# Optimization experiments

Measured on AMD Instinct MI355X. Metric: run time of the kernel, lower is better.

Reference implementation:

```python
import jax, jax.numpy as jnp
import numpy as np

V, D, N, DK, DV, H, DFF = 32000, 512, 6, 64, 64, 8, 2048
B, S = 8, 512
EPS = 1e-5


def _pe(seq_len, d_model):
    pos = np.arange(seq_len)[:, None].astype(np.float32)
    i = np.arange(0, d_model, 2).astype(np.float32)
    ang = pos / np.power(10000.0, i / d_model)
    pe = np.zeros((seq_len, d_model), dtype=np.float32)
    pe[:, 0::2] = np.sin(ang)
    pe[:, 1::2] = np.cos(ang)
    return jnp.asarray(pe)


def _ln(x, g, b):
    m = jnp.mean(x, axis=-1, keepdims=True)
    v = jnp.mean(jnp.square(x - m), axis=-1, keepdims=True)
    return (x - m) * jax.lax.rsqrt(v + EPS) * g + b


def _mha(xq, xkv, Wq, Wk, Wv, bq, bk, bv, mask):
    # Wq/Wk: [H,D,DK], Wv: [H,D,DV]; mask: [B,Sq,Skv] additive
    q = jnp.einsum('bsd,hdk->bhsk', xq, Wq) + bq[None, :, None, :]
    k = jnp.einsum('bsd,hdk->bhsk', xkv, Wk) + bk[None, :, None, :]
    v = jnp.einsum('bsd,hdk->bhsk', xkv, Wv) + bv[None, :, None, :]
    scores = jnp.einsum('bhqk,bhsk->bhqs', q, k) / jnp.sqrt(jnp.float32(DK))
    scores = scores + mask[:, None, :, :]
    attn = jax.nn.softmax(scores, axis=-1)
    out = jnp.einsum('bhqs,bhsv->bhqv', attn, v)  # [B,H,Sq,DV]
    return out.transpose(0, 2, 1, 3).reshape(xq.shape[0], xq.shape[1], H * DV)


def setup_inputs() -> dict:
    key = jax.random.key(0)
    ks = jax.random.split(key, 24)
    sc = 0.02
    inp = {
        'decoder_input': jax.random.randint(ks[0], (B, S), 0, V),
        'encoder_output': jax.random.normal(ks[1], (B, S, D), dtype=jnp.float32),
        'self_mask': jnp.where(jnp.tril(jnp.ones((S, S), dtype=bool)), 0.0, -1e9)[None].repeat(B, 0).astype(jnp.float32),
        'cross_mask': jnp.zeros((B, S, S), dtype=jnp.float32),
        'emb': jax.random.normal(ks[2], (V, D), dtype=jnp.float32),
        'Wq_s': jax.random.normal(ks[3], (N, H, D, DK)) * sc,
        'Wk_s': jax.random.normal(ks[4], (N, H, D, DK)) * sc,
        'Wv_s': jax.random.normal(ks[5], (N, H, D, DV)) * sc,
        'bq_s': jnp.zeros((N, H, DK)), 'bk_s': jnp.zeros((N, H, DK)), 'bv_s': jnp.zeros((N, H, DV)),
        'Wq_c': jax.random.normal(ks[6], (N, H, D, DK)) * sc,
        'Wk_c': jax.random.normal(ks[7], (N, H, D, DK)) * sc,
        'Wv_c': jax.random.normal(ks[8], (N, H, D, DV)) * sc,
        'bq_c': jnp.zeros((N, H, DK)), 'bk_c': jnp.zeros((N, H, DK)), 'bv_c': jnp.zeros((N, H, DV)),
        'W1': jax.random.normal(ks[9], (N, D, DFF)) * sc,
        'b1': jnp.zeros((N, DFF)),
        'W2': jax.random.normal(ks[10], (N, DFF, D)) * sc,
        'b2': jnp.zeros((N, D)),
        'ln1_g': jnp.ones((N, D)), 'ln1_b': jnp.zeros((N, D)),
        'ln2_g': jnp.ones((N, D)), 'ln2_b': jnp.zeros((N, D)),
    }
    return inp


def reference(decoder_input, encoder_output, self_mask, cross_mask, emb,
              Wq_s, Wk_s, Wv_s, bq_s, bk_s, bv_s,
              Wq_c, Wk_c, Wv_c, bq_c, bk_c, bv_c,
              W1, b1, W2, b2, ln1_g, ln1_b, ln2_g, ln2_b):
    x = emb[decoder_input] + _pe(decoder_input.shape[1], D)[None]
    for l in range(N):
        sa = _mha(x, x, Wq_s[l], Wk_s[l], Wv_s[l], bq_s[l], bk_s[l], bv_s[l], self_mask)
        x = _ln(x + sa, ln1_g[l], ln1_b[l])
        ca = _mha(x, encoder_output, Wq_c[l], Wk_c[l], Wv_c[l], bq_c[l], bk_c[l], bv_c[l], cross_mask)
        x = _ln(x + ca, ln2_g[l], ln2_b[l])
        ff = jax.nn.relu(jnp.einsum('bsd,df->bsf', x, W1[l]) + b1[l])
        ff = jnp.einsum('bsf,fd->bsd', ff, W2[l]) + b2[l]
        # source reuses layer_norm2 for the third norm (layer_norm3 is dead)
        x = _ln(x + ff, ln2_g[l], ln2_b[l])
    return x
```

## Files before the change

### kernel.cpp

```cpp
#include <hip/hip_runtime.h>
#include <hip/hip_bf16.h>
#include <math.h>

#define BB 8
#define SS 512
#define DDIM 512
#define HH 8
#define DFFV 2048
#define NLAYER 6
#define EPSV 1e-5f

typedef __attribute__((ext_vector_type(8))) short bf16x8;
typedef __attribute__((ext_vector_type(4))) float f32x4;

static __device__ __forceinline__ ushort f2bf(float f) {
  union { float f; unsigned u; } uf; uf.f = f;
  unsigned u = uf.u;
  unsigned r = (u + 0x7fffu + ((u >> 16) & 1u)) >> 16;
  return (ushort)r;
}
static __device__ __forceinline__ float bf2f(ushort h) {
  union { unsigned u; float f; } x;
  x.u = ((unsigned)h) << 16;
  return x.f;
}

static __device__ __forceinline__ void gload_lds16(const void* g, void* l) {
  __builtin_amdgcn_global_load_lds(
      (const __attribute__((address_space(1))) void*)g,
      (__attribute__((address_space(3))) void*)l, 16, 0, 0);
}

__global__ __launch_bounds__(256) void embed_pe_kernel(
    const int* __restrict__ idx, const float* __restrict__ emb,
    ushort* __restrict__ xb) {
  int t = blockIdx.x * blockDim.x + threadIdx.x;
  if (t >= BB * SS * DDIM) return;
  int d = t & (DDIM - 1);
  int bs = t >> 9;
  int s = bs & (SS - 1);
  int tok = idx[bs];
  int i2 = d & ~1;
  float ang = (float)s * powf(10000.0f, -((float)i2) / (float)DDIM);
  float pe = (d & 1) ? cosf(ang) : sinf(ang);
  float v = emb[tok * DDIM + d] + pe;
  xb[t] = f2bf(v);
}

__global__ __launch_bounds__(256) void cast_bf16_kernel(
    const float* __restrict__ in, ushort* __restrict__ out, int n4) {
  int t = blockIdx.x * blockDim.x + threadIdx.x;
  if (t >= n4) return;
  float4 v = reinterpret_cast<const float4*>(in)[t];
  ushort4 o;
  o.x = f2bf(v.x); o.y = f2bf(v.y); o.z = f2bf(v.z); o.w = f2bf(v.w);
  reinterpret_cast<ushort4*>(out)[t] = o;
}

__global__ __launch_bounds__(256) void wtrans_kernel(
    const float* __restrict__ in, ushort* __restrict__ out, int R, int C,
    int lgH, size_t zl) {
  __shared__ float t[32][33];
  int z = blockIdx.z;
  int l = z >> lgH, hh = z & ((1 << lgH) - 1);
  const float* ip = in + (size_t)z * R * C;
  ushort* op = out + (size_t)l * zl + (size_t)hh * R * C;
  int j = threadIdx.x & 31, i0 = threadIdx.x >> 5;
  int r0 = blockIdx.y * 32, c0 = blockIdx.x * 32;
#pragma unroll
  for (int p = 0; p < 4; p++) {
    int r = r0 + i0 + p * 8;
    t[i0 + p * 8][j] = ip[(size_t)r * C + c0 + j];
  }
  __syncthreads();
#pragma unroll
  for (int p = 0; p < 4; p++) {
    int cc = c0 + i0 + p * 8;
    op[(size_t)cc * R + r0 + j] = f2bf(t[j][i0 + p * 8]);
  }
}

__global__ __launch_bounds__(256) void pack_bias_kernel(
    const float* __restrict__ bq, const float* __restrict__ bk,
    const float* __restrict__ bv, const float* __restrict__ bkc,
    const float* __restrict__ bvc, float* __restrict__ qkvb,
    float* __restrict__ ckvb) {
  int t = blockIdx.x * 256 + threadIdx.x;
  if (t < NLAYER * 1536) {
    int l = t / 1536, n = t % 1536;
    float v = n < 512 ? bq[l * 512 + n]
                      : (n < 1024 ? bk[l * 512 + n - 512] : bv[l * 512 + n - 1024]);
    qkvb[t] = v;
  }
  if (t < NLAYER * 1024) {
    int l = t / 1024, n = t % 1024;
    ckvb[t] = n < 512 ? bkc[l * 512 + n] : bvc[l * 512 + n - 512];
  }
}

template <int BM, int BN, int RELU, int OUTBF, int NTV, int LGP, int SPLITK>
__global__ __launch_bounds__(256) void gemm_mfma(
    const ushort* __restrict__ A, const ushort* __restrict__ Bw,
    const float* __restrict__ bias, float* __restrict__ Cf,
    ushort* __restrict__ Cb, ushort* __restrict__ vt, int M, int N, int K) {
  constexpr int WM = BM / 64;
  constexpr int WN = 4 / WM;
  constexpr int W = BN / WN;
  constexpr int AF = 4;
  constexpr int BF = W / 16;
  constexpr int GA = BM * 8;
  constexpr int GPT = (BM + BN) * 8 / 256;
  __shared__ __align__(16) ushort lds_s[2][(BM + BN) * 64];
  int bn = blockIdx.x * BN, bm = blockIdx.y * BM;
  int kz = (SPLITK > 1) ? blockIdx.z : 0;
  int Keff = K / SPLITK;
  int kbase = kz * Keff;
  int tid = threadIdx.x, lane = tid & 63, w = tid >> 6;
  int wm = w / WN, wn = w % WN;
  int c = lane & 15, g16 = lane >> 4;
  f32x4 acc[AF][BF] = {};

  auto STAGE = [&](int k0, int bufi) {
#pragma unroll
    for (int i = 0; i < GPT; i++) {
      int gidx = i * 256 + tid;
      int gbase = (i * 4 + w) * 64;
      const ushort* src;
      if (gidx < GA) {
        int row = gidx >> 3, dg = gidx & 7;
        src = A + (size_t)(bm + row) * K + kbase + k0 + ((dg ^ (row & 7)) << 3);
      } else {
        int bidx = gidx - GA;
        int row = bidx >> 3, dg = bidx & 7;
        src = Bw + (size_t)(bn + row) * K + kbase + k0 + ((dg ^ (row & 7)) << 3);
      }
      gload_lds16(src, (void*)((char*)(&lds_s[bufi][0]) + gbase * 16));
    }
  };

  int nk = Keff >> 6;
  STAGE(0, 0);
  for (int kt = 0; kt < nk; kt++) {
    int cur = kt & 1;
    if (kt + 1 < nk) {
      STAGE((kt + 1) << 6, cur ^ 1);
      asm volatile("s_waitcnt vmcnt(%0)" ::"n"(GPT) : "memory");
    } else {
      asm volatile("s_waitcnt vmcnt(0)" ::: "memory");
    }
    __builtin_amdgcn_s_barrier();
    __builtin_amdgcn_sched_barrier(0);
    const ushort* Alds = &lds_s[cur][0];
    const ushort* Blds = &lds_s[cur][BM * 64];
#pragma unroll
    for (int ks = 0; ks < 2; ks++) {
      int g = ks * 4 + g16;
      bf16x8 a[AF], b[BF];
#pragma unroll
      for (int i = 0; i < AF; i++) {
        int R = wm * 64 + i * 16 + c;
        a[i] = *(const bf16x8*)(Alds + R * 64 + ((g ^ (R & 7)) << 3));
      }
#pragma unroll
      for (int j = 0; j < BF; j++) {
        int Rb = wn * W + j * 16 + c;
        b[j] = *(const bf16x8*)(Blds + Rb * 64 + ((g ^ (Rb & 7)) << 3));
      }
#pragma unroll
      for (int i = 0; i < AF; i++)
#pragma unroll
        for (int j = 0; j < BF; j++)
          acc[i][j] = __builtin_amdgcn_mfma_f32_16x16x32_bf16(a[i], b[j],
                                                              acc[i][j], 0, 0, 0);
    }
    __builtin_amdgcn_sched_barrier(0);
    __builtin_amdgcn_s_barrier();
  }
  int rb = g16 * 4;
#pragma unroll
  for (int j = 0; j < BF; j++) {
    int col = bn + wn * W + j * 16 + c;
    float bv = (SPLITK > 1 && kz != 0) ? 0.0f : bias[col];
    int cc = LGP ? (col & ((1 << LGP) - 1)) : col;
    int lp = LGP ? (col >> LGP) : 0;
    if (NTV > 0 && cc >= NTV) {
      int hh = (cc - NTV) >> 6, dv = col & 63;
      ushort* vtl = vt + (size_t)lp * 2097152;
#pragma unroll
      for (int i = 0; i < AF; i++) {
        int row = bm + wm * 64 + i * 16 + rb;
        int b_ = row >> 9, s_ = row & 511;
        ushort4 o4;
        o4.x = f2bf(acc[i][j][0] + bv);
        o4.y = f2bf(acc[i][j][1] + bv);
        o4.z = f2bf(acc[i][j][2] + bv);
        o4.w = f2bf(acc[i][j][3] + bv);
        *reinterpret_cast<ushort4*>(
            vtl + ((size_t)(b_ * 8 + hh) * 64 + dv) * 512 + s_) = o4;
      }
    } else {
#pragma unroll
      for (int i = 0; i < AF; i++) {
#pragma unroll
        for (int qq = 0; qq < 4; qq++) {
          int row = bm + wm * 64 + i * 16 + rb + qq;
          float v = acc[i][j][qq] + bv;
          if (RELU) v = fmaxf(v, 0.0f);
          if (OUTBF)
            Cb[(size_t)row * N + col] = f2bf(v);
          else
            Cf[(size_t)kz * M * N + (size_t)row * N + col] = v;
        }
      }
    }
  }
}

template <int MASKED, int NW>
__global__ __launch_bounds__(NW * 64) void attn_mfma(
    const ushort* __restrict__ q, int qstr, const ushort* __restrict__ k,
    int kstr, const ushort* __restrict__ vt, ushort* __restrict__ out) {
  __shared__ __align__(16) char lds[32768 + NW * 2048];
  int q0 = blockIdx.x * (NW * 16), h = blockIdx.y, b = blockIdx.z;
  int tid = threadIdx.x, lane = tid & 63, w = tid >> 6;
  int c = lane & 15, g16 = lane >> 4, rb = g16 * 4;

  bf16x8 qa[2];
#pragma unroll
  for (int ks = 0; ks < 2; ks++)
    qa[ks] = *(const bf16x8*)(q + (size_t)(b * SS + q0 + 16 * w + c) * qstr +
                              h * 64 + ks * 32 + g16 * 8);
  f32x4 o[4] = {};
  float mrow[4], lrow[4];
#pragma unroll
  for (int j = 0; j < 4; j++) { mrow[j] = -1e30f; lrow[j] = 0.f; }

  int nt = MASKED ? (q0 >> 6) + 1 : 8;
  int pbase = 32768 + w * 2048;

  constexpr int GPTK = 512 / (NW * 64);
  bf16x8 rk[GPTK], rv[GPTK];
  const ushort* vbase = vt + ((size_t)(b * 8 + h) * 64) * 512;
  auto LOADT = [&](int kv0) {
#pragma unroll
    for (int i = 0; i < GPTK; i++) {
      int idx = tid + i * (NW * 64);
      int row = idx >> 3, gw = idx & 7;
      rk[i] = *(const bf16x8*)(k + (size_t)(b * SS + kv0 + row) * kstr +
                               h * 64 + gw * 8);
      rv[i] = *(const bf16x8*)(vbase + (size_t)row * 512 + kv0 + gw * 8);
    }
  };
  auto WRT = [&](int bufi) {
    char* p = lds + bufi * 16384;
#pragma unroll
    for (int i = 0; i < GPTK; i++) {
      int idx = tid + i * (NW * 64);
      int row = idx >> 3, gw = idx & 7;
      *(bf16x8*)(p + row * 128 + ((gw ^ (row & 7)) << 4)) = rk[i];
      *(bf16x8*)(p + 8192 + row * 128 + ((gw ^ (row & 7)) << 4)) = rv[i];
    }
  };
  LOADT(0);
  WRT(0);
  for (int t = 0; t < nt; t++) {
    if (t + 1 < nt) LOADT((t + 1) * 64);
    __syncthreads();
    char* kb_ = lds + (t & 1) * 16384;
    char* vb_ = kb_ + 8192;
    f32x4 s[4] = {};
    __builtin_amdgcn_s_setprio(1);
#pragma unroll
    for (int ks = 0; ks < 2; ks++) {
      int g = ks * 4 + g16;
#pragma unroll
      for (int f = 0; f < 4; f++) {
        int row = f * 16 + c;
        bf16x8 k8 = *(bf16x8*)(kb_ + row * 128 + ((g ^ (row & 7)) << 4));
        s[f] = __builtin_amdgcn_mfma_f32_16x16x32_bf16(qa[ks], k8, s[f], 0, 0, 0);
      }
    }
    __builtin_amdgcn_s_setprio(0);
    if (MASKED && t == nt - 1) {
#pragma unroll
      for (int f = 0; f < 4; f++)
#pragma unroll
        for (int j = 0; j < 4; j++)
          s[f][j] = s[f][j] * 0.125f +
                    ((f * 16 + c) <= (16 * w + rb + j) ? 0.0f : -1e9f);
    } else {
#pragma unroll
      for (int f = 0; f < 4; f++)
#pragma unroll
        for (int j = 0; j < 4; j++) s[f][j] *= 0.125f;
    }
#pragma unroll
    for (int j = 0; j < 4; j++) {
      float tm = fmaxf(fmaxf(s[0][j], s[1][j]), fmaxf(s[2][j], s[3][j]));
      tm = fmaxf(tm, __shfl_xor(tm, 1));
      tm = fmaxf(tm, __shfl_xor(tm, 2));
      tm = fmaxf(tm, __shfl_xor(tm, 4));
      tm = fmaxf(tm, __shfl_xor(tm, 8));
      float mn = fmaxf(mrow[j], tm);
      float sc = __expf(mrow[j] - mn);
      float p0 = __expf(s[0][j] - mn), p1 = __expf(s[1][j] - mn);
      float p2 = __expf(s[2][j] - mn), p3 = __expf(s[3][j] - mn);
      s[0][j] = p0; s[1][j] = p1; s[2][j] = p2; s[3][j] = p3;
      float ps = p0 + p1 + p2 + p3;
      ps += __shfl_xor(ps, 1);
      ps += __shfl_xor(ps, 2);
      ps += __shfl_xor(ps, 4);
      ps += __shfl_xor(ps, 8);
      lrow[j] = lrow[j] * sc + ps;
      mrow[j] = mn;
      o[0][j] *= sc; o[1][j] *= sc; o[2][j] *= sc; o[3][j] *= sc;
    }
#pragma unroll
    for (int f = 0; f < 4; f++) {
      int col = f * 16 + c;
      int cg = col >> 3, cb2 = (col & 7) * 2;
#pragma unroll
      for (int j = 0; j < 4; j++) {
        int r = rb + j;
        *(ushort*)(lds + pbase + r * 128 + ((cg ^ (r & 7)) << 4) + cb2) =
            f2bf(s[f][j]);
      }
    }
    __builtin_amdgcn_s_setprio(1);
#pragma unroll
    for (int ks2 = 0; ks2 < 2; ks2++) {
      int g = ks2 * 4 + g16;
      bf16x8 pa = *(bf16x8*)(lds + pbase + c * 128 + ((g ^ (c & 7)) << 4));
#pragma unroll
      for (int f = 0; f < 4; f++) {
        int row = f * 16 + c;
        bf16x8 v8 = *(bf16x8*)(vb_ + row * 128 + ((g ^ (row & 7)) << 4));
        o[f] = __builtin_amdgcn_mfma_f32_16x16x32_bf16(pa, v8, o[f], 0, 0, 0);
      }
    }
    __builtin_amdgcn_s_setprio(0);
    if (t + 1 < nt) WRT((t + 1) & 1);
  }
#pragma unroll
  for (int j = 0; j < 4; j++) {
    float inv = 1.0f / lrow[j];
    size_t rowo = (size_t)(b * SS + q0 + 16 * w + rb + j) * 512 + h * 64;
#pragma unroll
    for (int f = 0; f < 4; f++)
      out[rowo + f * 16 + c] = f2bf(o[f][j] * inv);
  }
}

template <int Y2>
__global__ __launch_bounds__(256) void add_ln_kernel(
    ushort* __restrict__ xb, const ushort* __restrict__ yb,
    const float* __restrict__ y0, const float* __restrict__ y1,
    const float* __restrict__ g, const float* __restrict__ bta,
    float* __restrict__ xf) {
  int row = blockIdx.x * 4 + (threadIdx.x >> 6);
  int lane = threadIdx.x & 63;
  int base = row * DDIM + lane * 8;
  bf16x8 xv = *reinterpret_cast<const bf16x8*>(xb + base);
  float v[8];
  if (Y2) {
    float4 a0 = *reinterpret_cast<const float4*>(y0 + base);
    float4 a1 = *reinterpret_cast<const float4*>(y0 + base + 4);
    float4 c0 = *reinterpret_cast<const float4*>(y1 + base);
    float4 c1 = *reinterpret_cast<const float4*>(y1 + base + 4);
    v[0] = bf2f((ushort)xv[0]) + a0.x + c0.x;
    v[1] = bf2f((ushort)xv[1]) + a0.y + c0.y;
    v[2] = bf2f((ushort)xv[2]) + a0.z + c0.z;
    v[3] = bf2f((ushort)xv[3]) + a0.w + c0.w;
    v[4] = bf2f((ushort)xv[4]) + a1.x + c1.x;
    v[5] = bf2f((ushort)xv[5]) + a1.y + c1.y;
    v[6] = bf2f((ushort)xv[6]) + a1.z + c1.z;
    v[7] = bf2f((ushort)xv[7]) + a1.w + c1.w;
  } else {
    bf16x8 yv = *reinterpret_cast<const bf16x8*>(yb + base);
#pragma unroll
    for (int i = 0; i < 8; i++)
      v[i] = bf2f((ushort)xv[i]) + bf2f((ushort)yv[i]);
  }
  float s = 0.f;
#pragma unroll
  for (int i = 0; i < 8; i++) s += v[i];
#pragma unroll
  for (int off = 32; off > 0; off >>= 1) s += __shfl_xor(s, off);
  float mean = s * (1.0f / DDIM);
  float t2 = 0.f;
#pragma unroll
  for (int i = 0; i < 8; i++) {
    v[i] -= mean;
    t2 += v[i] * v[i];
  }
#pragma unroll
  for (int off = 32; off > 0; off >>= 1) t2 += __shfl_xor(t2, off);
  float rs = rsqrtf(t2 * (1.0f / DDIM) + EPSV);
  int cidx = lane * 8;
  float4 g0 = *reinterpret_cast<const float4*>(g + cidx);
  float4 g1 = *reinterpret_cast<const float4*>(g + cidx + 4);
  float4 b0 = *reinterpret_cast<const float4*>(bta + cidx);
  float4 b1 = *reinterpret_cast<const float4*>(bta + cidx + 4);
  float o[8];
  o[0] = v[0] * rs * g0.x + b0.x; o[1] = v[1] * rs * g0.y + b0.y;
  o[2] = v[2] * rs * g0.z + b0.z; o[3] = v[3] * rs * g0.w + b0.w;
  o[4] = v[4] * rs * g1.x + b1.x; o[5] = v[5] * rs * g1.y + b1.y;
  o[6] = v[6] * rs * g1.z + b1.z; o[7] = v[7] * rs * g1.w + b1.w;
  bf16x8 ob;
#pragma unroll
  for (int i = 0; i < 8; i++) ob[i] = (short)f2bf(o[i]);
  *reinterpret_cast<bf16x8*>(xb + base) = ob;
  if (xf) {
    float4 w0 = {o[0], o[1], o[2], o[3]}, w1 = {o[4], o[5], o[6], o[7]};
    *reinterpret_cast<float4*>(xf + base) = w0;
    *reinterpret_cast<float4*>(xf + base + 4) = w1;
  }
}

extern "C" void kernel_launch(void* const* d_in, const int* in_sizes, int n_in,
                              void* d_out, int out_size, void* d_ws,
                              size_t ws_size, hipStream_t stream) {
  const int* dec = (const int*)d_in[0];
  const float* enc = (const float*)d_in[1];
  const float* emb = (const float*)d_in[4];
  const float* Wq_s = (const float*)d_in[5];
  const float* Wk_s = (const float*)d_in[6];
  const float* Wv_s = (const float*)d_in[7];
  const float* bq_s = (const float*)d_in[8];
  const float* bk_s = (const float*)d_in[9];
  const float* bv_s = (const float*)d_in[10];
  const float* Wq_c = (const float*)d_in[11];
  const float* Wk_c = (const float*)d_in[12];
  const float* Wv_c = (const float*)d_in[13];
  const float* bq_c = (const float*)d_in[14];
  const float* bk_c = (const float*)d_in[15];
  const float* bv_c = (const float*)d_in[16];
  const float* W1 = (const float*)d_in[17];
  const float* b1 = (const float*)d_in[18];
  const float* W2 = (const float*)d_in[19];
  const float* b2 = (const float*)d_in[20];
  const float* ln1_g = (const float*)d_in[21];
  const float* ln1_b = (const float*)d_in[22];
  const float* ln2_g = (const float*)d_in[23];
  const float* ln2_b = (const float*)d_in[24];

  char* ws = (char*)d_ws;
  ushort* wqkv = (ushort*)(ws + 0);
  ushort* wqc = (ushort*)(ws + 9437184ull);
  ushort* wckv = (ushort*)(ws + 12582912ull);
  ushort* w1t = (ushort*)(ws + 18874368ull);
  ushort* w2t = (ushort*)(ws + 31457280ull);
  ushort* encb = (ushort*)(ws + 44040192ull);
  ushort* xb = (ushort*)(ws + 48234496ull);
  ushort* tmpb = (ushort*)(ws + 52428800ull);
  float* tmpf = (float*)(ws + 56623104ull);
  ushort* qkvbuf = (ushort*)(ws + 73400320ull);
  ushort* cq = (ushort*)(ws + 73400320ull);
  ushort* ff1b = (ushort*)(ws + 73400320ull);
  ushort* vt = (ushort*)(ws + 85983232ull);
  float* qkvbias = (float*)(ws + 90177536ull);
  float* ckvbias = (float*)(ws + 90214400ull);
  ushort* ckvbuf = (ushort*)(ws + 90238976ull);
  ushort* vtc = (ushort*)(ws + 140570624ull);

  const int M = BB * SS;
  dim3 g256(256);

  embed_pe_kernel<<<dim3((M * DDIM + 255) / 256), g256, 0, stream>>>(dec, emb,
                                                                     xb);
  cast_bf16_kernel<<<dim3(M * DDIM / 4 / 256), g256, 0, stream>>>(
      enc, encb, M * DDIM / 4);
  pack_bias_kernel<<<dim3(36), g256, 0, stream>>>(bq_s, bk_s, bv_s, bk_c, bv_c,
                                                  qkvbias, ckvbias);

  wtrans_kernel<<<dim3(2, 16, 48), g256, 0, stream>>>(Wq_s, wqkv, 512, 64, 3,
                                                      786432ull);
  wtrans_kernel<<<dim3(2, 16, 48), g256, 0, stream>>>(Wk_s, wqkv + 262144, 512,
                                                      64, 3, 786432ull);
  wtrans_kernel<<<dim3(2, 16, 48), g256, 0, stream>>>(Wv_s, wqkv + 524288, 512,
                                                      64, 3, 786432ull);
  wtrans_kernel<<<dim3(2, 16, 48), g256, 0, stream>>>(Wq_c, wqc, 512, 64, 3,
                                                      262144ull);
  wtrans_kernel<<<dim3(2, 16, 48), g256, 0, stream>>>(Wk_c, wckv, 512, 64, 3,
                                                      524288ull);
  wtrans_kernel<<<dim3(2, 16, 48), g256, 0, stream>>>(Wv_c, wckv + 262144, 512,
                                                      64, 3, 524288ull);
  wtrans_kernel<<<dim3(64, 16, 6), g256, 0, stream>>>(W1, w1t, 512, 2048, 0,
                                                      1048576ull);
  wtrans_kernel<<<dim3(16, 64, 6), g256, 0, stream>>>(W2, w2t, 2048, 512, 0,
                                                      1048576ull);

  gemm_mfma<128, 128, 0, 1, 512, 10, 1><<<dim3(48, 32), g256, 0, stream>>>(
      encb, wckv, ckvbias, nullptr, ckvbuf, vtc, M, 6144, 512);

  for (int l = 0; l < NLAYER; l++) {
    gemm_mfma<64, 128, 0, 1, 1024, 0, 1><<<dim3(12, 64), g256, 0, stream>>>(
        xb, wqkv + (size_t)l * 786432, qkvbias + l * 1536, nullptr, qkvbuf, vt,
        M, 1536, 512);
    attn_mfma<1, 4><<<dim3(8, 8, 8), g256, 0, stream>>>(
        qkvbuf, 1536, qkvbuf + 512, 1536, vt, tmpb);
    add_ln_kernel<0><<<dim3(M / 4), g256, 0, stream>>>(
        xb, tmpb, nullptr, nullptr, ln1_g + l * 512, ln1_b + l * 512, nullptr);
    gemm_mfma<64, 64, 0, 1, 0, 0, 1><<<dim3(8, 64), g256, 0, stream>>>(
        xb, wqc + (size_t)l * 262144, bq_c + l * 512, nullptr, cq, nullptr, M,
        512, 512);
    attn_mfma<0, 8><<<dim3(4, 8, 8), dim3(512), 0, stream>>>(
        cq, 512, ckvbuf + l * 1024, 6144, vtc + (size_t)l * 2097152, tmpb);
    add_ln_kernel<0><<<dim3(M / 4), g256, 0, stream>>>(
        xb, tmpb, nullptr, nullptr, ln2_g + l * 512, ln2_b + l * 512, nullptr);
    gemm_mfma<128, 128, 1, 1, 0, 0, 1><<<dim3(16, 32), g256, 0, stream>>>(
        xb, w1t + (size_t)l * 1048576, b1 + l * DFFV, nullptr, ff1b, nullptr,
        M, DFFV, 512);
    gemm_mfma<128, 64, 0, 0, 0, 0, 2><<<dim3(8, 32, 2), g256, 0, stream>>>(
        ff1b, w2t + (size_t)l * 1048576, b2 + l * 512, tmpf, nullptr, nullptr,
        M, 512, DFFV);
    add_ln_kernel<1><<<dim3(M / 4), g256, 0, stream>>>(
        xb, nullptr, tmpf, tmpf + (size_t)M * 512, ln2_g + l * 512,
        ln2_b + l * 512, (l == NLAYER - 1) ? (float*)d_out : nullptr);
  }
}
```

Baseline: 733.1 us.

## Fold softmax scale into Q weights, transpose score MFMA, swizzle GEMM workgroups

Pre-multiplies the Q projection weights and biases by log2(e)/sqrt(dk) so attention can use exp2 directly with no per-score scaling. The score MFMA operands are swapped so each lane holds one query row, which collapses the row max/sum reductions to two cross-lane shuffles and allows packed ushort4 stores of P into LDS. GEMM workgroups are also remapped with an XCD-style swizzle of the block index to improve cache locality across the chiplets. Rounding Q weights to bf16 after scaling slightly changes numerics, and the per-row rescale now needs extra shuffles to broadcast the factors.

```diff
diff --git a/kernel.cpp b/kernel.cpp
--- a/kernel.cpp
+++ b/kernel.cpp
@@ -9,6 +9,7 @@
 #define DFFV 2048
 #define NLAYER 6
 #define EPSV 1e-5f
+#define WQS 0.180336880f
 
 typedef __attribute__((ext_vector_type(8))) short bf16x8;
 typedef __attribute__((ext_vector_type(4))) float f32x4;
@@ -59,7 +60,7 @@
 
 __global__ __launch_bounds__(256) void wtrans_kernel(
     const float* __restrict__ in, ushort* __restrict__ out, int R, int C,
-    int lgH, size_t zl) {
+    int lgH, size_t zl, float scale) {
   __shared__ float t[32][33];
   int z = blockIdx.z;
   int l = z >> lgH, hh = z & ((1 << lgH) - 1);
@@ -76,19 +77,20 @@
 #pragma unroll
   for (int p = 0; p < 4; p++) {
     int cc = c0 + i0 + p * 8;
-    op[(size_t)cc * R + r0 + j] = f2bf(t[j][i0 + p * 8]);
+    op[(size_t)cc * R + r0 + j] = f2bf(t[j][i0 + p * 8] * scale);
   }
 }
 
 __global__ __launch_bounds__(256) void pack_bias_kernel(
     const float* __restrict__ bq, const float* __restrict__ bk,
     const float* __restrict__ bv, const float* __restrict__ bkc,
-    const float* __restrict__ bvc, float* __restrict__ qkvb,
-    float* __restrict__ ckvb) {
+    const float* __restrict__ bvc, const float* __restrict__ bqc,
+    float* __restrict__ qkvb, float* __restrict__ ckvb,
+    float* __restrict__ cqb) {
   int t = blockIdx.x * 256 + threadIdx.x;
   if (t < NLAYER * 1536) {
     int l = t / 1536, n = t % 1536;
-    float v = n < 512 ? bq[l * 512 + n]
+    float v = n < 512 ? bq[l * 512 + n] * WQS
                       : (n < 1024 ? bk[l * 512 + n - 512] : bv[l * 512 + n - 1024]);
     qkvb[t] = v;
   }
@@ -96,6 +98,7 @@
     int l = t / 1024, n = t % 1024;
     ckvb[t] = n < 512 ? bkc[l * 512 + n] : bvc[l * 512 + n - 512];
   }
+  if (t < NLAYER * 512) cqb[t] = bqc[t] * WQS;
 }
 
 template <int BM, int BN, int RELU, int OUTBF, int NTV, int LGP, int SPLITK>
@@ -111,7 +114,11 @@
   constexpr int GA = BM * 8;
   constexpr int GPT = (BM + BN) * 8 / 256;
   __shared__ __align__(16) ushort lds_s[2][(BM + BN) * 64];
-  int bn = blockIdx.x * BN, bm = blockIdx.y * BM;
+  int nwg = gridDim.x * gridDim.y;
+  int wg = blockIdx.y * gridDim.x + blockIdx.x;
+  int cpx = nwg >> 3;
+  int swz = (wg & 7) * cpx + (wg >> 3);
+  int bn = (swz % gridDim.x) * BN, bm = (swz / gridDim.x) * BM;
   int kz = (SPLITK > 1) ? blockIdx.z : 0;
   int Keff = K / SPLITK;
   int kbase = kz * Keff;
@@ -231,9 +238,7 @@
     qa[ks] = *(const bf16x8*)(q + (size_t)(b * SS + q0 + 16 * w + c) * qstr +
                               h * 64 + ks * 32 + g16 * 8);
   f32x4 o[4] = {};
-  float mrow[4], lrow[4];
-#pragma unroll
-  for (int j = 0; j < 4; j++) { mrow[j] = -1e30f; lrow[j] = 0.f; }
+  float mq = -1e30f, lq = 0.f;
 
   int nt = MASKED ? (q0 >> 6) + 1 : 8;
   int pbase = 32768 + w * 2048;
@@ -268,7 +273,7 @@
     __syncthreads();
     char* kb_ = lds + (t & 1) * 16384;
     char* vb_ = kb_ + 8192;
-    f32x4 s[4] = {};
+    f32x4 sp[4] = {};
     __builtin_amdgcn_s_setprio(1);
 #pragma unroll
     for (int ks = 0; ks < 2; ks++) {
@@ -277,54 +282,54 @@
       for (int f = 0; f < 4; f++) {
         int row = f * 16 + c;
         bf16x8 k8 = *(bf16x8*)(kb_ + row * 128 + ((g ^ (row & 7)) << 4));
-        s[f] = __builtin_amdgcn_mfma_f32_16x16x32_bf16(qa[ks], k8, s[f], 0, 0, 0);
+        sp[f] = __builtin_amdgcn_mfma_f32_16x16x32_bf16(k8, qa[ks], sp[f], 0, 0, 0);
       }
     }
     __builtin_amdgcn_s_setprio(0);
     if (MASKED && t == nt - 1) {
+      int ql = 16 * w + c;
 #pragma unroll
       for (int f = 0; f < 4; f++)
 #pragma unroll
         for (int j = 0; j < 4; j++)
-          s[f][j] = s[f][j] * 0.125f +
-                    ((f * 16 + c) <= (16 * w + rb + j) ? 0.0f : -1e9f);
-    } else {
-#pragma unroll
-      for (int f = 0; f < 4; f++)
-#pragma unroll
-        for (int j = 0; j < 4; j++) s[f][j] *= 0.125f;
-    }
+          sp[f][j] += (f * 16 + rb + j) <= ql ? 0.0f : -1e9f;
+    }
+    float tmax = -1e30f;
+#pragma unroll
+    for (int f = 0; f < 4; f++)
+#pragma unroll
+      for (int j = 0; j < 4; j++) tmax = fmaxf(tmax, sp[f][j]);
+    tmax = fmaxf(tmax, __shfl_xor(tmax, 16));
+    tmax = fmaxf(tmax, __shfl_xor(tmax, 32));
+    float mn = fmaxf(mq, tmax);
+    float scq = exp2f(mq - mn);
+    float psum = 0.f;
+#pragma unroll
+    for (int f = 0; f < 4; f++)
+#pragma unroll
+      for (int j = 0; j < 4; j++) {
+        float pv = exp2f(sp[f][j] - mn);
+        sp[f][j] = pv;
+        psum += pv;
+      }
+    psum += __shfl_xor(psum, 16);
+    psum += __shfl_xor(psum, 32);
+    lq = lq * scq + psum;
+    mq = mn;
+    int sb = lane & 48;
 #pragma unroll
     for (int j = 0; j < 4; j++) {
-      float tm = fmaxf(fmaxf(s[0][j], s[1][j]), fmaxf(s[2][j], s[3][j]));
-      tm = fmaxf(tm, __shfl_xor(tm, 1));
-      tm = fmaxf(tm, __shfl_xor(tm, 2));
-      tm = fmaxf(tm, __shfl_xor(tm, 4));
-      tm = fmaxf(tm, __shfl_xor(tm, 8));
-      float mn = fmaxf(mrow[j], tm);
-      float sc = __expf(mrow[j] - mn);
-      float p0 = __expf(s[0][j] - mn), p1 = __expf(s[1][j] - mn);
-      float p2 = __expf(s[2][j] - mn), p3 = __expf(s[3][j] - mn);
-      s[0][j] = p0; s[1][j] = p1; s[2][j] = p2; s[3][j] = p3;
-      float ps = p0 + p1 + p2 + p3;
-      ps += __shfl_xor(ps, 1);
-      ps += __shfl_xor(ps, 2);
-      ps += __shfl_xor(ps, 4);
-      ps += __shfl_xor(ps, 8);
-      lrow[j] = lrow[j] * sc + ps;
-      mrow[j] = mn;
-      o[0][j] *= sc; o[1][j] *= sc; o[2][j] *= sc; o[3][j] *= sc;
+      float scj = __shfl(scq, sb | (rb + j));
+      o[0][j] *= scj; o[1][j] *= scj; o[2][j] *= scj; o[3][j] *= scj;
     }
 #pragma unroll
     for (int f = 0; f < 4; f++) {
-      int col = f * 16 + c;
-      int cg = col >> 3, cb2 = (col & 7) * 2;
-#pragma unroll
-      for (int j = 0; j < 4; j++) {
-        int r = rb + j;
-        *(ushort*)(lds + pbase + r * 128 + ((cg ^ (r & 7)) << 4) + cb2) =
-            f2bf(s[f][j]);
-      }
+      int kv0 = f * 16 + rb;
+      ushort4 pk;
+      pk.x = f2bf(sp[f][0]); pk.y = f2bf(sp[f][1]);
+      pk.z = f2bf(sp[f][2]); pk.w = f2bf(sp[f][3]);
+      int gg = kv0 >> 3, off = (kv0 & 7) * 2;
+      *(ushort4*)(lds + pbase + c * 128 + (((gg) ^ (c & 7)) << 4) + off) = pk;
     }
     __builtin_amdgcn_s_setprio(1);
 #pragma unroll
@@ -341,13 +346,15 @@
     __builtin_amdgcn_s_setprio(0);
     if (t + 1 < nt) WRT((t + 1) & 1);
   }
+  float invq = 1.0f / lq;
+  int sb = lane & 48;
 #pragma unroll
   for (int j = 0; j < 4; j++) {
-    float inv = 1.0f / lrow[j];
+    float invj = __shfl(invq, sb | (rb + j));
     size_t rowo = (size_t)(b * SS + q0 + 16 * w + rb + j) * 512 + h * 64;
 #pragma unroll
     for (int f = 0; f < 4; f++)
-      out[rowo + f * 16 + c] = f2bf(o[f][j] * inv);
+      out[rowo + f * 16 + c] = f2bf(o[f][j] * invj);
   }
 }
 
@@ -462,6 +469,7 @@
   float* ckvbias = (float*)(ws + 90214400ull);
   ushort* ckvbuf = (ushort*)(ws + 90238976ull);
   ushort* vtc = (ushort*)(ws + 140570624ull);
+  float* cqbias = (float*)(ws + 165736448ull);
 
   const int M = BB * SS;
   dim3 g256(256);
@@ -471,24 +479,25 @@
   cast_bf16_kernel<<<dim3(M * DDIM / 4 / 256), g256, 0, stream>>>(
       enc, encb, M * DDIM / 4);
   pack_bias_kernel<<<dim3(36), g256, 0, stream>>>(bq_s, bk_s, bv_s, bk_c, bv_c,
-                                                  qkvbias, ckvbias);
+                                                  bq_c, qkvbias, ckvbias,
+                                                  cqbias);
 
   wtrans_kernel<<<dim3(2, 16, 48), g256, 0, stream>>>(Wq_s, wqkv, 512, 64, 3,
-                                                      786432ull);
+                                                      786432ull, WQS);
   wtrans_kernel<<<dim3(2, 16, 48), g256, 0, stream>>>(Wk_s, wqkv + 262144, 512,
-                                                      64, 3, 786432ull);
+                                                      64, 3, 786432ull, 1.0f);
   wtrans_kernel<<<dim3(2, 16, 48), g256, 0, stream>>>(Wv_s, wqkv + 524288, 512,
-                                                      64, 3, 786432ull);
+                                                      64, 3, 786432ull, 1.0f);
   wtrans_kernel<<<dim3(2, 16, 48), g256, 0, stream>>>(Wq_c, wqc, 512, 64, 3,
-                                                      262144ull);
+                                                      262144ull, WQS);
   wtrans_kernel<<<dim3(2, 16, 48), g256, 0, stream>>>(Wk_c, wckv, 512, 64, 3,
-                                                      524288ull);
+                                                      524288ull, 1.0f);
   wtrans_kernel<<<dim3(2, 16, 48), g256, 0, stream>>>(Wv_c, wckv + 262144, 512,
-                                                      64, 3, 524288ull);
+                                                      64, 3, 524288ull, 1.0f);
   wtrans_kernel<<<dim3(64, 16, 6), g256, 0, stream>>>(W1, w1t, 512, 2048, 0,
-                                                      1048576ull);
+                                                      1048576ull, 1.0f);
   wtrans_kernel<<<dim3(16, 64, 6), g256, 0, stream>>>(W2, w2t, 2048, 512, 0,
-                                                      1048576ull);
+                                                      1048576ull, 1.0f);
 
   gemm_mfma<128, 128, 0, 1, 512, 10, 1><<<dim3(48, 32), g256, 0, stream>>>(
       encb, wckv, ckvbias, nullptr, ckvbuf, vtc, M, 6144, 512);
@@ -502,8 +511,8 @@
     add_ln_kernel<0><<<dim3(M / 4), g256, 0, stream>>>(
         xb, tmpb, nullptr, nullptr, ln1_g + l * 512, ln1_b + l * 512, nullptr);
     gemm_mfma<64, 64, 0, 1, 0, 0, 1><<<dim3(8, 64), g256, 0, stream>>>(
-        xb, wqc + (size_t)l * 262144, bq_c + l * 512, nullptr, cq, nullptr, M,
-        512, 512);
+        xb, wqc + (size_t)l * 262144, cqbias + l * 512, nullptr, cq, nullptr,
+        M, 512, 512);
     attn_mfma<0, 8><<<dim3(4, 8, 8), dim3(512), 0, stream>>>(
         cq, 512, ckvbuf + l * 1024, 6144, vtc + (size_t)l * 2097152, tmpb);
     add_ln_kernel<0><<<dim3(M / 4), g256, 0, stream>>>(
```

After: 643.6 us. 12.2% less time.
